# Kernel optimization log

Hardware: AMD Instinct MI355X
Metric: run time of the kernel (lower is better)

Reference implementation:

```python
import jax, jax.numpy as jnp
import numpy as np

N_NODES = 50000
IN_CH = 128
OUT_CH = 64
N_EDGES = 800000


def setup_inputs() -> dict:
    key = jax.random.key(0)
    k_x, k_e, k_w, k_b = jax.random.split(key, 4)
    x = jax.random.normal(k_x, (N_NODES, IN_CH), dtype=jnp.float32)
    edge_index = jax.random.randint(k_e, (2, N_EDGES), 0, N_NODES, dtype=jnp.int64)
    # nn.Linear(in, out, bias=False): weight [out, in], applied as x @ W^T
    W = jax.random.normal(k_w, (OUT_CH, IN_CH), dtype=jnp.float32) * (1.0 / np.sqrt(IN_CH))
    bias = jax.random.normal(k_b, (OUT_CH,), dtype=jnp.float32) * 0.02
    return {"x": x, "edge_index": edge_index, "W": W, "bias": bias}


def reference(x, edge_index, W, bias):
    # linear projection (no bias): [N, in] @ [in, out] -> [N, out]
    h = x @ W.T
    src = edge_index[0]
    dst = edge_index[1]
    # gather source node feats per edge: [E, out]
    msgs = h[src]
    # scatter_add into dest nodes: [N, out]
    out = jax.ops.segment_sum(msgs, dst, num_segments=h.shape[0])
    return out + bias
```

## Files before the change

kernel.cpp:

```cpp
#include <hip/hip_runtime.h>

#define IN_CH 128
#define OUT_CH 64
#define TN 256
#define KC 32
#define XS 36
#define WS_STRIDE 129

#define PBLOCKS 512
#define NB 800
#define CAPA 8
#define DCAP 32
#define OCAP 64

__device__ __forceinline__ unsigned f2bf(float f) {
    unsigned u = __float_as_uint(f);
    return (u + 0x7FFFu + ((u >> 16) & 1u)) >> 16;
}

__device__ __forceinline__ void fma4(float4& acc, float s, const float4& wv) {
    acc.x += s * wv.x;
    acc.y += s * wv.y;
    acc.z += s * wv.z;
    acc.w += s * wv.w;
}

__global__ __launch_bounds__(256) void k_fusedA(const float* __restrict__ x,
                                                const float* __restrict__ W,
                                                unsigned* __restrict__ h16,
                                                const int* __restrict__ ei,
                                                unsigned* __restrict__ cells,
                                                uint2* __restrict__ spill,
                                                int* __restrict__ spillCount,
                                                int nNodes, int nEdges, int gemmBlocks) {
    __shared__ float smem[TN * XS + IN_CH * OUT_CH];
    __shared__ int is64s;
    int tid = threadIdx.x;
    int i = blockIdx.x;

    if (i >= gemmBlocks) {
        int pid = i - gemmBlocks;
        unsigned* lists = (unsigned*)smem;
        int* curs = (int*)smem + NB * CAPA;
        for (int k = tid; k < NB; k += 256) curs[k] = 0;
        if (tid == 0) {
            int v = 1;
#pragma unroll
            for (int j = 0; j < 16; ++j)
                if (ei[2 * j + 1] != 0) v = 0;
            is64s = v;
        }
        __syncthreads();
        int is64 = is64s;

        int chunk = (nEdges + PBLOCKS - 1) / PBLOCKS;
        int e0 = pid * chunk;
        int e1 = min(e0 + chunk, nEdges);
        for (int e = e0 + tid; e < e1; e += 256) {
            int src, dst;
            if (is64) {
                src = ((const int2*)ei)[e].x;
                dst = ((const int2*)ei)[nEdges + e].x;
            } else {
                src = ei[e];
                dst = ei[nEdges + e];
            }
            if ((unsigned)src >= (unsigned)nNodes) src = 0;
            if ((unsigned)dst >= (unsigned)nNodes) dst = 0;
            int bucket = dst >> 6;
            int rank = (bucket < NB) ? atomicAdd(&curs[bucket], 1) : CAPA;
            if (rank < CAPA) {
                lists[bucket * CAPA + rank] = (unsigned)src | ((unsigned)(dst & 63) << 16);
            } else {
                int sp = atomicAdd(spillCount, 1);
                if (sp < nEdges) spill[sp] = make_uint2((unsigned)src, (unsigned)dst);
            }
        }
        __syncthreads();

        size_t base = (size_t)pid * NB;
        uint4* cells4 = (uint4*)(cells + base * CAPA);
        for (int j = tid; j < NB * CAPA / 4; j += 256) {
            uint4 v = *(const uint4*)(lists + 4 * j);
            if ((j & 1) == 0) {
                int cell = j >> 1;
                v.x = (v.x & 0x0FFFFFFFu) | ((unsigned)min(curs[cell], CAPA) << 28);
            }
            cells4[j] = v;
        }
        return;
    }

    float* u  = smem;
    float* wt = smem + TN * XS;
    int nodeBase = i * TN;
    int remRows = nNodes - nodeBase;
    if (remRows > TN) remRows = TN;

    {
        const float4* W4 = (const float4*)W;
        for (int j = tid; j < IN_CH * OUT_CH / 4; j += 256) {
            float4 v = W4[j];
            int o = j >> 5;
            int k = (j & 31) * 4;
            float* d = u + o * WS_STRIDE + k;
            d[0] = v.x; d[1] = v.y; d[2] = v.z; d[3] = v.w;
        }
    }
    __syncthreads();
    {
        int o = tid & 63;
        int k0 = (tid >> 6) * 32;
#pragma unroll 8
        for (int k = k0; k < k0 + 32; ++k)
            wt[k * OUT_CH + o] = u[o * WS_STRIDE + k];
    }
    __syncthreads();

    int lane = tid & 63;
    int wv   = tid >> 6;
    int cb   = (lane & 7) * 8;
    int ng   = lane >> 3;

    float4 acc[8][2];
#pragma unroll
    for (int q = 0; q < 8; ++q) {
        acc[q][0] = make_float4(0.f, 0.f, 0.f, 0.f);
        acc[q][1] = make_float4(0.f, 0.f, 0.f, 0.f);
    }

    for (int c = 0; c < 4; ++c) {
        {
            const float* xb = x + (size_t)nodeBase * IN_CH + c * KC;
#pragma unroll
            for (int r = 0; r < 8; ++r) {
                int f  = tid + 256 * r;
                int nd = f >> 3;
                int j4 = (f & 7) * 4;
                float4 v = make_float4(0.f, 0.f, 0.f, 0.f);
                if (nd < remRows) v = *(const float4*)(xb + (size_t)nd * IN_CH + j4);
                *(float4*)(u + nd * XS + j4) = v;
            }
        }
        __syncthreads();

#pragma unroll
        for (int kc = 0; kc < KC; kc += 4) {
            int kg = c * KC + kc;
            float4 a[8];
#pragma unroll
            for (int q = 0; q < 8; ++q)
                a[q] = *(const float4*)(u + (wv * 64 + ng + 8 * q) * XS + kc);
#pragma unroll
            for (int kk = 0; kk < 4; ++kk) {
                float4 w0 = *(const float4*)(wt + (kg + kk) * OUT_CH + cb);
                float4 w1 = *(const float4*)(wt + (kg + kk) * OUT_CH + cb + 4);
#pragma unroll
                for (int q = 0; q < 8; ++q) {
                    float s = (kk == 0) ? a[q].x : (kk == 1) ? a[q].y : (kk == 2) ? a[q].z : a[q].w;
                    fma4(acc[q][0], s, w0);
                    fma4(acc[q][1], s, w1);
                }
            }
        }
        __syncthreads();
    }

#pragma unroll
    for (int q = 0; q < 8; ++q) {
        int n = nodeBase + wv * 64 + ng + 8 * q;
        if (n < nNodes) {
            uint4 pk;
            pk.x = f2bf(acc[q][0].x) | (f2bf(acc[q][0].y) << 16);
            pk.y = f2bf(acc[q][0].z) | (f2bf(acc[q][0].w) << 16);
            pk.z = f2bf(acc[q][1].x) | (f2bf(acc[q][1].y) << 16);
            pk.w = f2bf(acc[q][1].z) | (f2bf(acc[q][1].w) << 16);
            *(uint4*)(h16 + (size_t)n * 32 + (lane & 7) * 4) = pk;
        }
    }
}

__global__ __launch_bounds__(512, 8) void k_fusedB(const unsigned* __restrict__ cells,
                                                   const unsigned* __restrict__ h16,
                                                   const float* __restrict__ bias,
                                                   float* __restrict__ out,
                                                   const uint2* __restrict__ spill,
                                                   const int* __restrict__ spillCount,
                                                   int nNodes, int nEdges) {
    __shared__ unsigned nl[64 * DCAP];
    __shared__ int nc[64];
    __shared__ unsigned oS[OCAP];
    __shared__ int ocnt;
    int tid = threadIdx.x;
    int b = blockIdx.x;
    int nodeBase = b * 64;

    if (tid < 64) nc[tid] = 0;
    if (tid == 0) ocnt = 0;
    __syncthreads();

    if (b < NB) {
        for (int blk = tid; blk < PBLOCKS; blk += 512) {
            const unsigned* cb = cells + ((size_t)blk * NB + b) * CAPA;
            uint4 w0 = *(const uint4*)(cb + 0);
            uint4 w1 = *(const uint4*)(cb + 4);
            int c = (int)(w0.x >> 28);
            if (c > CAPA) c = CAPA;
            unsigned w[CAPA] = {w0.x, w0.y, w0.z, w0.w, w1.x, w1.y, w1.z, w1.w};
#pragma unroll
            for (int r = 0; r < CAPA; ++r) {
                if (r < c) {
                    unsigned rec = w[r];
                    int sub = (int)(rec >> 16) & 63;
                    int rank = atomicAdd(&nc[sub], 1);
                    if (rank < DCAP) {
                        nl[sub * DCAP + rank] = rec & 0xFFFFu;
                    } else {
                        int rk = atomicAdd(&ocnt, 1);
                        if (rk < OCAP) oS[rk] = (rec & 0xFFFFu) | ((unsigned)sub << 16);
                    }
                }
            }
        }
    }

    {
        int sc = *spillCount;
        if (sc > nEdges) sc = nEdges;
        for (int e = tid; e < sc; e += 512) {
            uint2 sd = spill[e];
            if ((int)(sd.y >> 6) == b) {
                int sub = (int)(sd.y & 63);
                int rank = atomicAdd(&nc[sub], 1);
                if (rank < DCAP) {
                    nl[sub * DCAP + rank] = sd.x;
                } else {
                    int rk = atomicAdd(&ocnt, 1);
                    if (rk < OCAP) oS[rk] = sd.x | ((unsigned)sub << 16);
                }
            }
        }
    }
    __syncthreads();

    int lane = tid & 63;
    int wv   = tid >> 6;
    int q4   = lane >> 4;
    int cp   = lane & 15;
    float4 bv = *(const float4*)(bias + cp * 4);
    int oc = ocnt;
    if (oc > OCAP) oc = OCAP;

#pragma unroll
    for (int q = 0; q < 8; ++q) {
        int sub = wv * 8 + q;
        int node = nodeBase + sub;
        if (node >= nNodes) continue;

        int d = nc[sub];
        if (d > DCAP) d = DCAP;
        int base = sub * DCAP;

        float4 acc = {0.f, 0.f, 0.f, 0.f};
        for (int j = 0; j < d; j += 16) {
            int i0 = j + q4;
            int i1 = i0 + 4;
            int i2 = i0 + 8;
            int i3 = i0 + 12;
            int s0 = (int)nl[base + (i0 < d ? i0 : 0)];
            int s1 = (int)nl[base + (i1 < d ? i1 : 0)];
            int s2 = (int)nl[base + (i2 < d ? i2 : 0)];
            int s3 = (int)nl[base + (i3 < d ? i3 : 0)];
            uint2 v0 = *(const uint2*)(h16 + (size_t)s0 * 32 + cp * 2);
            uint2 v1 = *(const uint2*)(h16 + (size_t)s1 * 32 + cp * 2);
            uint2 v2 = *(const uint2*)(h16 + (size_t)s2 * 32 + cp * 2);
            uint2 v3 = *(const uint2*)(h16 + (size_t)s3 * 32 + cp * 2);
            if (i0 >= d) { v0.x = 0u; v0.y = 0u; }
            if (i1 >= d) { v1.x = 0u; v1.y = 0u; }
            if (i2 >= d) { v2.x = 0u; v2.y = 0u; }
            if (i3 >= d) { v3.x = 0u; v3.y = 0u; }
            acc.x += __uint_as_float(v0.x << 16);
            acc.y += __uint_as_float(v0.x & 0xFFFF0000u);
            acc.z += __uint_as_float(v0.y << 16);
            acc.w += __uint_as_float(v0.y & 0xFFFF0000u);
            acc.x += __uint_as_float(v1.x << 16);
            acc.y += __uint_as_float(v1.x & 0xFFFF0000u);
            acc.z += __uint_as_float(v1.y << 16);
            acc.w += __uint_as_float(v1.y & 0xFFFF0000u);
            acc.x += __uint_as_float(v2.x << 16);
            acc.y += __uint_as_float(v2.x & 0xFFFF0000u);
            acc.z += __uint_as_float(v2.y << 16);
            acc.w += __uint_as_float(v2.y & 0xFFFF0000u);
            acc.x += __uint_as_float(v3.x << 16);
            acc.y += __uint_as_float(v3.x & 0xFFFF0000u);
            acc.z += __uint_as_float(v3.y << 16);
            acc.w += __uint_as_float(v3.y & 0xFFFF0000u);
        }

        for (int t = 0; t < oc; ++t) {
            unsigned rec = oS[t];
            if ((int)(rec >> 16) == sub && q4 == 0) {
                int s = (int)(rec & 0xFFFFu);
                uint2 v = *(const uint2*)(h16 + (size_t)s * 32 + cp * 2);
                acc.x += __uint_as_float(v.x << 16);
                acc.y += __uint_as_float(v.x & 0xFFFF0000u);
                acc.z += __uint_as_float(v.y << 16);
                acc.w += __uint_as_float(v.y & 0xFFFF0000u);
            }
        }

        acc.x += __shfl_down(acc.x, 32, 64);
        acc.y += __shfl_down(acc.y, 32, 64);
        acc.z += __shfl_down(acc.z, 32, 64);
        acc.w += __shfl_down(acc.w, 32, 64);
        acc.x += __shfl_down(acc.x, 16, 64);
        acc.y += __shfl_down(acc.y, 16, 64);
        acc.z += __shfl_down(acc.z, 16, 64);
        acc.w += __shfl_down(acc.w, 16, 64);
        if (lane < 16) {
            float4 o;
            o.x = acc.x + bv.x;
            o.y = acc.y + bv.y;
            o.z = acc.z + bv.z;
            o.w = acc.w + bv.w;
            *(float4*)(out + (size_t)node * OUT_CH + cp * 4) = o;
        }
    }
}

extern "C" void kernel_launch(void* const* d_in, const int* in_sizes, int n_in,
                              void* d_out, int out_size, void* d_ws, size_t ws_size,
                              hipStream_t stream) {
    const float* x    = (const float*)d_in[0];
    const int*   ei   = (const int*)d_in[1];
    const float* W    = (const float*)d_in[2];
    const float* bias = (const float*)d_in[3];
    float* out = (float*)d_out;

    int nNodes = in_sizes[0] / IN_CH;
    int nEdges = in_sizes[1] / 2;
    int gemmBlocks = (nNodes + TN - 1) / TN;
    int realBuckets = (nNodes + 63) / 64;
    int totalBlocks = gemmBlocks + PBLOCKS;

    char* p = (char*)d_ws;
    auto alloc = [&](size_t bytes) {
        char* r = p;
        p += (bytes + 255) & ~(size_t)255;
        return r;
    };
    unsigned* h16        = (unsigned*)alloc((size_t)nNodes * 32 * sizeof(unsigned));
    unsigned* cells      = (unsigned*)alloc((size_t)PBLOCKS * NB * CAPA * sizeof(unsigned));
    uint2*    spill      = (uint2*)alloc((size_t)nEdges * sizeof(uint2));
    int*      spillCount = (int*)alloc(sizeof(int));

    hipMemsetAsync(spillCount, 0, sizeof(int), stream);
    k_fusedA<<<totalBlocks, 256, 0, stream>>>(x, W, h16, ei, cells,
                                              spill, spillCount, nNodes, nEdges, gemmBlocks);
    k_fusedB<<<realBuckets, 512, 0, stream>>>(cells, h16, bias, out,
                                              spill, spillCount, nNodes, nEdges);
}
```

Baseline: 142.4 us.

## Interleave partition and GEMM blocks, transpose cell layout, use bf16 weights in LDS

Reduces the fused GEMM block to 128 threads and 128 rows, and stores W transposed as bf16 in shared memory, dropping the intermediate staging transpose and shrinking LDS use. Edge-partition blocks are now spread evenly among GEMM blocks instead of trailing them, so the two kinds of work share the GPU concurrently. The cell buffer layout is transposed to [bucket][pblock], so the consumer kernel reads contiguous memory per bucket. Rounding W to bf16 adds a little error to the projection.

```diff
diff --git a/kernel.cpp b/kernel.cpp
--- a/kernel.cpp
+++ b/kernel.cpp
@@ -2,10 +2,8 @@
 
 #define IN_CH 128
 #define OUT_CH 64
-#define TN 256
-#define KC 32
+#define TN 128
 #define XS 36
-#define WS_STRIDE 129
 
 #define PBLOCKS 512
 #define NB 800
@@ -25,24 +23,36 @@
     acc.w += s * wv.w;
 }
 
-__global__ __launch_bounds__(256) void k_fusedA(const float* __restrict__ x,
+__device__ __forceinline__ float4 bf2f4(uint2 p) {
+    float4 r;
+    r.x = __uint_as_float(p.x << 16);
+    r.y = __uint_as_float(p.x & 0xFFFF0000u);
+    r.z = __uint_as_float(p.y << 16);
+    r.w = __uint_as_float(p.y & 0xFFFF0000u);
+    return r;
+}
+
+__global__ __launch_bounds__(128) void k_fusedA(const float* __restrict__ x,
                                                 const float* __restrict__ W,
                                                 unsigned* __restrict__ h16,
                                                 const int* __restrict__ ei,
                                                 unsigned* __restrict__ cells,
                                                 uint2* __restrict__ spill,
                                                 int* __restrict__ spillCount,
-                                                int nNodes, int nEdges, int gemmBlocks) {
-    __shared__ float smem[TN * XS + IN_CH * OUT_CH];
+                                                int nNodes, int nEdges, int totalBlocks) {
+    __shared__ __align__(16) float smem[TN * XS + IN_CH * OUT_CH / 2];
     __shared__ int is64s;
     int tid = threadIdx.x;
+
     int i = blockIdx.x;
-
-    if (i >= gemmBlocks) {
-        int pid = i - gemmBlocks;
+    long long t = (long long)i * PBLOCKS;
+    int pid = (int)(t / totalBlocks);
+    int isPartA = (int)((t + PBLOCKS) / totalBlocks) > pid;
+
+    if (isPartA) {
         unsigned* lists = (unsigned*)smem;
         int* curs = (int*)smem + NB * CAPA;
-        for (int k = tid; k < NB; k += 256) curs[k] = 0;
+        for (int k = tid; k < NB; k += 128) curs[k] = 0;
         if (tid == 0) {
             int v = 1;
 #pragma unroll
@@ -56,7 +66,7 @@
         int chunk = (nEdges + PBLOCKS - 1) / PBLOCKS;
         int e0 = pid * chunk;
         int e1 = min(e0 + chunk, nEdges);
-        for (int e = e0 + tid; e < e1; e += 256) {
+        for (int e = e0 + tid; e < e1; e += 128) {
             int src, dst;
             if (is64) {
                 src = ((const int2*)ei)[e].x;
@@ -78,49 +88,39 @@
         }
         __syncthreads();
 
-        size_t base = (size_t)pid * NB;
-        uint4* cells4 = (uint4*)(cells + base * CAPA);
-        for (int j = tid; j < NB * CAPA / 4; j += 256) {
-            uint4 v = *(const uint4*)(lists + 4 * j);
-            if ((j & 1) == 0) {
-                int cell = j >> 1;
-                v.x = (v.x & 0x0FFFFFFFu) | ((unsigned)min(curs[cell], CAPA) << 28);
-            }
-            cells4[j] = v;
+        for (int cell = tid; cell < NB; cell += 128) {
+            uint4 v0 = *(const uint4*)(lists + cell * CAPA);
+            uint4 v1 = *(const uint4*)(lists + cell * CAPA + 4);
+            v0.x = (v0.x & 0x0FFFFFFFu) | ((unsigned)min(curs[cell], CAPA) << 28);
+            uint4* dst4 = (uint4*)(cells + ((size_t)cell * PBLOCKS + pid) * CAPA);
+            dst4[0] = v0;
+            dst4[1] = v1;
         }
         return;
     }
 
-    float* u  = smem;
-    float* wt = smem + TN * XS;
-    int nodeBase = i * TN;
+    int gid = i - pid;
+    float* u = smem;
+    unsigned short* wt16 = (unsigned short*)(smem + TN * XS);
+    int nodeBase = gid * TN;
     int remRows = nNodes - nodeBase;
     if (remRows > TN) remRows = TN;
 
     {
         const float4* W4 = (const float4*)W;
-        for (int j = tid; j < IN_CH * OUT_CH / 4; j += 256) {
-            float4 v = W4[j];
-            int o = j >> 5;
-            int k = (j & 31) * 4;
-            float* d = u + o * WS_STRIDE + k;
-            d[0] = v.x; d[1] = v.y; d[2] = v.z; d[3] = v.w;
-        }
-    }
-    __syncthreads();
-    {
-        int o = tid & 63;
-        int k0 = (tid >> 6) * 32;
-#pragma unroll 8
-        for (int k = k0; k < k0 + 32; ++k)
-            wt[k * OUT_CH + o] = u[o * WS_STRIDE + k];
-    }
-    __syncthreads();
-
-    int lane = tid & 63;
-    int wv   = tid >> 6;
-    int cb   = (lane & 7) * 8;
-    int ng   = lane >> 3;
+        for (int f = tid; f < IN_CH * OUT_CH / 4; f += 128) {
+            float4 v = W4[f];
+            int o  = f >> 5;
+            int k4 = (f & 31) * 4;
+            wt16[(k4 + 0) * OUT_CH + o] = (unsigned short)f2bf(v.x);
+            wt16[(k4 + 1) * OUT_CH + o] = (unsigned short)f2bf(v.y);
+            wt16[(k4 + 2) * OUT_CH + o] = (unsigned short)f2bf(v.z);
+            wt16[(k4 + 3) * OUT_CH + o] = (unsigned short)f2bf(v.w);
+        }
+    }
+
+    int tx  = tid & 7;
+    int tyg = tid >> 3;
 
     float4 acc[8][2];
 #pragma unroll
@@ -130,11 +130,12 @@
     }
 
     for (int c = 0; c < 4; ++c) {
+        __syncthreads();
         {
-            const float* xb = x + (size_t)nodeBase * IN_CH + c * KC;
+            const float* xb = x + (size_t)nodeBase * IN_CH + c * 32;
 #pragma unroll
             for (int r = 0; r < 8; ++r) {
-                int f  = tid + 256 * r;
+                int f  = tid + 128 * r;
                 int nd = f >> 3;
                 int j4 = (f & 7) * 4;
                 float4 v = make_float4(0.f, 0.f, 0.f, 0.f);
@@ -145,16 +146,17 @@
         __syncthreads();
 
 #pragma unroll
-        for (int kc = 0; kc < KC; kc += 4) {
-            int kg = c * KC + kc;
+        for (int kc = 0; kc < 32; kc += 4) {
             float4 a[8];
 #pragma unroll
             for (int q = 0; q < 8; ++q)
-                a[q] = *(const float4*)(u + (wv * 64 + ng + 8 * q) * XS + kc);
+                a[q] = *(const float4*)(u + (tyg + 16 * q) * XS + kc);
 #pragma unroll
             for (int kk = 0; kk < 4; ++kk) {
-                float4 w0 = *(const float4*)(wt + (kg + kk) * OUT_CH + cb);
-                float4 w1 = *(const float4*)(wt + (kg + kk) * OUT_CH + cb + 4);
+                int kg = c * 32 + kc + kk;
+                uint4 wp = *(const uint4*)(wt16 + kg * OUT_CH + tx * 8);
+                float4 w0 = bf2f4(make_uint2(wp.x, wp.y));
+                float4 w1 = bf2f4(make_uint2(wp.z, wp.w));
 #pragma unroll
                 for (int q = 0; q < 8; ++q) {
                     float s = (kk == 0) ? a[q].x : (kk == 1) ? a[q].y : (kk == 2) ? a[q].z : a[q].w;
@@ -163,19 +165,18 @@
                 }
             }
         }
-        __syncthreads();
     }
 
 #pragma unroll
     for (int q = 0; q < 8; ++q) {
-        int n = nodeBase + wv * 64 + ng + 8 * q;
+        int n = nodeBase + tyg + 16 * q;
         if (n < nNodes) {
             uint4 pk;
             pk.x = f2bf(acc[q][0].x) | (f2bf(acc[q][0].y) << 16);
             pk.y = f2bf(acc[q][0].z) | (f2bf(acc[q][0].w) << 16);
             pk.z = f2bf(acc[q][1].x) | (f2bf(acc[q][1].y) << 16);
             pk.w = f2bf(acc[q][1].z) | (f2bf(acc[q][1].w) << 16);
-            *(uint4*)(h16 + (size_t)n * 32 + (lane & 7) * 4) = pk;
+            *(uint4*)(h16 + (size_t)n * 32 + tx * 4) = pk;
         }
     }
 }
@@ -201,7 +202,7 @@
 
     if (b < NB) {
         for (int blk = tid; blk < PBLOCKS; blk += 512) {
-            const unsigned* cb = cells + ((size_t)blk * NB + b) * CAPA;
+            const unsigned* cb = cells + ((size_t)b * PBLOCKS + blk) * CAPA;
             uint4 w0 = *(const uint4*)(cb + 0);
             uint4 w1 = *(const uint4*)(cb + 4);
             int c = (int)(w0.x >> 28);
@@ -355,8 +356,8 @@
     int*      spillCount = (int*)alloc(sizeof(int));
 
     hipMemsetAsync(spillCount, 0, sizeof(int), stream);
-    k_fusedA<<<totalBlocks, 256, 0, stream>>>(x, W, h16, ei, cells,
-                                              spill, spillCount, nNodes, nEdges, gemmBlocks);
+    k_fusedA<<<totalBlocks, 128, 0, stream>>>(x, W, h16, ei, cells,
+                                              spill, spillCount, nNodes, nEdges, totalBlocks);
     k_fusedB<<<realBuckets, 512, 0, stream>>>(cells, h16, bias, out,
                                               spill, spillCount, nNodes, nEdges);
 }
```

New measurement: 146.8 us. 3.1% more time.
